# Optimization experiments

Hardware: AMD Instinct MI355X
Metric: run time of the kernel (lower is better)

The kernel has to match this reference:

```python
import jax, jax.numpy as jnp
import numpy as np

ALPHA = 0.2
SIGMA_REC = 0.15
B, T, N, IN, OUT, MASK_LEN = 256, 750, 512, 6, 2, 250


def setup_inputs() -> dict:
    key = jax.random.key(0)
    k_u, k_noise, k_rec, k_in, k_out, k_mask = jax.random.split(key, 6)
    noise_scale = np.sqrt(2.0 * ALPHA * SIGMA_REC ** 2).astype(np.float32)
    return {
        "u": jax.random.normal(k_u, (B, T, IN), dtype=jnp.float32),
        "noise": noise_scale * jax.random.normal(k_noise, (B, T, N), dtype=jnp.float32),
        "w_rec": jax.random.normal(k_rec, (N, N), dtype=jnp.float32) / np.float32(np.sqrt(N)),
        "w_in": jax.random.normal(k_in, (N, IN), dtype=jnp.float32) / np.float32(np.sqrt(IN)),
        "w_out": jax.random.normal(k_out, (OUT, N), dtype=jnp.float32) / np.float32(np.sqrt(N)),
        "mask": jnp.sort(jax.random.randint(k_mask, (MASK_LEN,), 0, T)),
    }


def _run_rnn(u, noise, w_rec, w_in):
    # u: [B,T,IN], noise: [B,T,N]; leaky ReLU RNN, t-1 update steps.
    b, t, _ = u.shape
    n = w_rec.shape[0]
    # Precompute input drive for all steps: [T-1, B, N]
    drive = jnp.einsum('bti,ni->tbn', u[:, : t - 1], w_in) + jnp.swapaxes(noise[:, : t - 1], 0, 1)

    def step(h, d):
        h_new = (1.0 - ALPHA) * h + ALPHA * jax.nn.relu(h @ w_rec.T + d)
        return h_new, h_new

    h0 = jnp.zeros((b, n), dtype=u.dtype)
    _, hs = jax.lax.scan(step, h0, drive)            # [T-1, B, N]
    states = jnp.concatenate([h0[None], hs], axis=0)  # [T, B, N]
    return jnp.swapaxes(states, 0, 1)                 # [B, T, N]


def reference(u, noise, w_rec, w_in, w_out, mask):
    states = _run_rnn(u, noise, w_rec, w_in)
    out = jnp.einsum('btn,on->bto', states, w_out)  # output_layer(states)
    return states, out[:, mask, :], out
```

## Files before the change

### kernel.cpp

```cpp
#include <hip/hip_runtime.h>
#include <hip/hip_bf16.h>


typedef __attribute__((ext_vector_type(4))) float f32x4;
typedef __attribute__((ext_vector_type(8))) short s16x8;

constexpr int BB = 256, TT = 750, NN = 512, INN = 6, OUTN = 2, MLEN = 250;
constexpr int BBLK = 16;
constexpr int NBLKS = BB / BBLK;
constexpr int WPB = 8;
constexpr int NSL = NN / WPB;
constexpr int NREG = 46;
constexpr int NLDSF = 18;
constexpr int HBYTES = BBLK * NN * 2;
constexpr int WOFF = HBYTES;
constexpr int SMEM_BYTES = WOFF + WPB * NLDSF * 1024;
constexpr int DRVELTS = NBLKS * WPB * 64 * 16;

__device__ __forceinline__ unsigned short f2bf(float f) {
    unsigned v = __float_as_uint(f);
    v += 0x7fffu + ((v >> 16) & 1u);
    return (unsigned short)(v >> 16);
}
__device__ __forceinline__ float bf2f(unsigned short h) {
    return __uint_as_float(((unsigned)h) << 16);
}

__global__ __launch_bounds__(256)
void drive_kernel(const float* __restrict__ u, const float* __restrict__ noise,
                  const float* __restrict__ w_in, unsigned short* __restrict__ drv)
{
    int gid = blockIdx.x * 256 + threadIdx.x;
    int t = gid >> 13;
    if (t >= TT - 1) return;
    int lane = gid & 63, w = (gid >> 6) & 7, blk = (gid >> 9) & 15;
    int qq = lane >> 4, lr = lane & 15;

    float wv[4][INN];
    #pragma unroll
    for (int tt = 0; tt < 4; ++tt) {
        int n = w * NSL + 16 * tt + lr;
        #pragma unroll
        for (int i = 0; i < INN; ++i) wv[tt][i] = w_in[n * INN + i];
    }
    alignas(16) unsigned short o[16];
    #pragma unroll
    for (int r = 0; r < 4; ++r) {
        int b = blk * BBLK + 4 * qq + r;
        const float* up = u + ((size_t)b * TT + t) * INN;
        float uv[INN];
        #pragma unroll
        for (int i = 0; i < INN; ++i) uv[i] = up[i];
        const float* np = noise + ((size_t)b * TT + t) * NN;
        #pragma unroll
        for (int tt = 0; tt < 4; ++tt) {
            int n = w * NSL + 16 * tt + lr;
            float d = np[n];
            #pragma unroll
            for (int i = 0; i < INN; ++i) d += uv[i] * wv[tt][i];
            o[tt * 4 + r] = f2bf(d);
        }
    }
    s16x8* dst = (s16x8*)(drv + (size_t)gid * 16);
    dst[0] = *(const s16x8*)&o[0];
    dst[1] = *(const s16x8*)&o[8];
}

__global__ __launch_bounds__(512, 2)
void rnn_scan_kernel(const float* __restrict__ w_rec,
                     const unsigned short* __restrict__ drv,
                     float* __restrict__ states)
{
    extern __shared__ char smem[];
    const int tid = threadIdx.x;
    const int w = tid >> 6, lane = tid & 63;
    const int qq = lane >> 4, lr = lane & 15, p7 = lr & 7;
    const int blk = blockIdx.x;
    const int bg = blk * BBLK;

    s16x8 breg[NREG];
    #pragma unroll
    for (int tt = 0; tt < 4; ++tt) {
        #pragma unroll
        for (int kk = 0; kk < 16; ++kk) {
            const int f = tt * 16 + kk;
            const int n = w * NSL + 16 * tt + lr;
            const float* p = w_rec + (size_t)n * NN + 32 * kk + 8 * qq;
            f32x4 x0 = *(const f32x4*)p;
            f32x4 x1 = *(const f32x4*)(p + 4);
            union { s16x8 v; unsigned short s[8]; } fr;
            #pragma unroll
            for (int j = 0; j < 4; ++j) { fr.s[j] = f2bf(x0[j]); fr.s[4+j] = f2bf(x1[j]); }
            if (f < NREG) breg[f] = fr.v;
            else *(s16x8*)(smem + WOFF + (w * NLDSF + (f - NREG)) * 1024 + lane * 16) = fr.v;
        }
    }
    for (int i = tid; i < HBYTES / 4; i += 512) ((unsigned*)smem)[i] = 0u;
    for (int i = tid; i < BBLK * NN; i += 512)
        states[(size_t)(bg + (i >> 9)) * TT * NN + (i & 511)] = 0.f;
    __syncthreads();

    float stl[16];
    #pragma unroll
    for (int i = 0; i < 16; ++i) stl[i] = 0.f;

    const int rb64 = (p7 & 4) << 4;
    const int hbase0 = lr * 1024 + ((qq ^ (p7 & 3)) << 4);
    const char* hbE = smem + hbase0 + rb64;
    const char* hbO = smem + hbase0 - rb64;
    const char* wbase = smem + WOFF + w * (NLDSF * 1024) + lane * 16;

    const int s0 = 8 * w + (lr >> 3);
    const unsigned LB = 4096u * qq + ((unsigned)(s0 ^ (4 * (qq & 1))) << 4) + 2 * (lr & 7);

    float* rowp[4];
    #pragma unroll
    for (int r = 0; r < 4; ++r)
        rowp[r] = states + ((size_t)(bg + 4 * qq + r) * TT + 1) * NN + w * NSL + lr;

    const unsigned short* dptr = drv + ((size_t)(blk * WPB + w) * 64 + lane) * 16;

    for (int s = 1; s < TT; ++s) {
        const s16x8* dp = (const s16x8*)dptr;
        s16x8 dv0 = dp[0], dv1 = dp[1];
        dptr += DRVELTS;

        f32x4 a0 = {0.f,0.f,0.f,0.f}, a1 = a0, a2 = a0, a3 = a0;
        #pragma unroll
        for (int kk = 0; kk < 16; ++kk) {
            s16x8 av = *(const s16x8*)(((kk & 1) ? hbO : hbE) + (kk << 6));
            a0 = __builtin_amdgcn_mfma_f32_16x16x32_bf16(av, breg[kk],      a0, 0,0,0);
            a1 = __builtin_amdgcn_mfma_f32_16x16x32_bf16(av, breg[16 + kk], a1, 0,0,0);
            if (kk < 14)
                a2 = __builtin_amdgcn_mfma_f32_16x16x32_bf16(av, breg[32+kk], a2, 0,0,0);
            else
                a2 = __builtin_amdgcn_mfma_f32_16x16x32_bf16(
                         av, *(const s16x8*)(wbase + ((kk - 14) << 10)), a2, 0, 0, 0);
            a3 = __builtin_amdgcn_mfma_f32_16x16x32_bf16(
                     av, *(const s16x8*)(wbase + ((2 + kk) << 10)), a3, 0, 0, 0);
        }

        union { s16x8 v; unsigned short e[8]; } U0, U1;
        U0.v = dv0; U1.v = dv1;
        const f32x4 aX[4] = {a0, a1, a2, a3};
        float hnv[4][4];
        #pragma unroll
        for (int tt = 0; tt < 4; ++tt) {
            #pragma unroll
            for (int r = 0; r < 4; ++r) {
                float d = bf2f(tt < 2 ? U0.e[tt * 4 + r] : U1.e[(tt - 2) * 4 + r]);
                float pre = aX[tt][r] + d;
                float hn = 0.8f * stl[tt * 4 + r] + 0.2f * fmaxf(pre, 0.f);
                stl[tt * 4 + r] = hn;
                hnv[tt][r] = hn;
                __builtin_nontemporal_store(hn, rowp[r] + tt * 16);
            }
        }
        unsigned pk[8];
        #pragma unroll
        for (int p = 0; p < 2; ++p)
            #pragma unroll
            for (int r = 0; r < 4; ++r) {
                __hip_bfloat162 h2 = __float22bfloat162_rn(
                    make_float2(hnv[2 * p][r], hnv[2 * p + 1][r]));
                pk[p * 4 + r] = *reinterpret_cast<unsigned*>(&h2);
            }
        #pragma unroll
        for (int r = 0; r < 4; ++r) rowp[r] += NN;

        asm volatile("s_waitcnt lgkmcnt(0)\n\ts_barrier" ::: "memory");

        #pragma unroll
        for (int tt = 0; tt < 4; ++tt) {
            #pragma unroll
            for (int r = 0; r < 4; ++r) {
                const unsigned C = (unsigned)(((2 * tt) ^ r) << 4);
                unsigned short hv = (tt & 1) ? (unsigned short)(pk[(tt >> 1) * 4 + r] >> 16)
                                             : (unsigned short)(pk[(tt >> 1) * 4 + r]);
                *(unsigned short*)(smem + ((LB ^ C) + 1024 * r)) = hv;
            }
        }
        asm volatile("s_waitcnt lgkmcnt(0)\n\ts_barrier" ::: "memory");
    }
}

__global__ __launch_bounds__(256)
void proj_kernel(const float* __restrict__ states, const float* __restrict__ w_out,
                 float* __restrict__ outf)
{
    const int wv   = (blockIdx.x * blockDim.x + threadIdx.x) >> 6;
    const int lane = threadIdx.x & 63;
    const float* sp = states + (size_t)wv * NN + lane * 8;
    const float* w0 = w_out + lane * 8;
    const float* w1 = w_out + NN + lane * 8;
    float d0 = 0.f, d1 = 0.f;
    #pragma unroll
    for (int i = 0; i < 8; ++i) {
        float sv = sp[i];
        d0 += sv * w0[i];
        d1 += sv * w1[i];
    }
    #pragma unroll
    for (int off = 32; off > 0; off >>= 1) {
        d0 += __shfl_xor(d0, off);
        d1 += __shfl_xor(d1, off);
    }
    if (lane == 0) {
        outf[(size_t)wv * 2]     = d0;
        outf[(size_t)wv * 2 + 1] = d1;
    }
}

__global__ void mask_kernel(const int* __restrict__ mask, const float* __restrict__ outf,
                            float* __restrict__ outm)
{
    int idx = blockIdx.x * blockDim.x + threadIdx.x;
    if (idx >= BB * MLEN * OUTN) return;
    int o  = idx % OUTN;
    int jm = (idx / OUTN) % MLEN;
    int b  = idx / (OUTN * MLEN);
    int t  = mask[jm];
    outm[idx] = outf[((size_t)b * TT + t) * OUTN + o];
}

extern "C" void kernel_launch(void* const* d_in, const int* in_sizes, int n_in,
                              void* d_out, int out_size, void* d_ws, size_t ws_size,
                              hipStream_t stream)
{
    (void)in_sizes; (void)n_in; (void)out_size; (void)ws_size;
    const float* u     = (const float*)d_in[0];
    const float* noise = (const float*)d_in[1];
    const float* w_rec = (const float*)d_in[2];
    const float* w_in  = (const float*)d_in[3];
    const float* w_out = (const float*)d_in[4];
    const int*   mask  = (const int*)d_in[5];

    float* states = (float*)d_out;
    float* outm   = states + (size_t)BB * TT * NN;
    float* outf   = outm + (size_t)BB * MLEN * OUTN;

    unsigned short* drvpk = (unsigned short*)d_ws;

    hipFuncSetAttribute((const void*)rnn_scan_kernel,
                        hipFuncAttributeMaxDynamicSharedMemorySize, SMEM_BYTES);

    drive_kernel<<<(TT - 1) * 32, 256, 0, stream>>>(u, noise, w_in, drvpk);
    rnn_scan_kernel<<<NBLKS, 512, SMEM_BYTES, stream>>>(w_rec, drvpk, states);
    proj_kernel<<<(BB * TT) / 4, 256, 0, stream>>>(states, w_out, outf);
    mask_kernel<<<(BB * MLEN * OUTN + 255) / 256, 256, 0, stream>>>(mask, outf, outm);
}
```

Measured before the change: 1.833 ms.

## Fuse output projection into RNN scan with per-warp partials and reduce kernel

Computes the w_out projection inside the recurrent scan from the freshly computed hidden states. Each wavefront reduces across its 16 lanes with DPP and writes per-wave partial sums to the workspace, and a small reduce kernel sums the 8 partials into the output. This removes the separate proj_kernel, which re-read the full states tensor of about 390 MB from memory. In exchange it adds ALU, DPP and store work to the serial time-step loop and needs a workspace large enough for the partials, falling back to the old path when the workspace is too small.

Measured after the change: 2.280 ms. 24.4% more time.

```diff
diff --git a/kernel.cpp b/kernel.cpp
--- a/kernel.cpp
+++ b/kernel.cpp
@@ -3,6 +3,7 @@
 
 
 typedef __attribute__((ext_vector_type(4))) float f32x4;
+typedef __attribute__((ext_vector_type(2))) float f32x2;
 typedef __attribute__((ext_vector_type(8))) short s16x8;
 
 constexpr int BB = 256, TT = 750, NN = 512, INN = 6, OUTN = 2, MLEN = 250;
@@ -16,6 +17,8 @@
 constexpr int WOFF = HBYTES;
 constexpr int SMEM_BYTES = WOFF + WPB * NLDSF * 1024;
 constexpr int DRVELTS = NBLKS * WPB * 64 * 16;
+constexpr size_t DRVTOT = (size_t)(TT - 1) * DRVELTS;
+constexpr size_t PARTN = (size_t)WPB * BB * TT * OUTN;
 
 __device__ __forceinline__ unsigned short f2bf(float f) {
     unsigned v = __float_as_uint(f);
@@ -25,6 +28,12 @@
 __device__ __forceinline__ float bf2f(unsigned short h) {
     return __uint_as_float(((unsigned)h) << 16);
 }
+
+#define DPPRED(v)                                                                 \
+    v += __int_as_float(__builtin_amdgcn_mov_dpp(__float_as_int(v), 0x128, 0xF, 0xF, false)); \
+    v += __int_as_float(__builtin_amdgcn_mov_dpp(__float_as_int(v), 0x124, 0xF, 0xF, false)); \
+    v += __int_as_float(__builtin_amdgcn_mov_dpp(__float_as_int(v), 0x122, 0xF, 0xF, false)); \
+    v += __int_as_float(__builtin_amdgcn_mov_dpp(__float_as_int(v), 0x121, 0xF, 0xF, false));
 
 __global__ __launch_bounds__(256)
 void drive_kernel(const float* __restrict__ u, const float* __restrict__ noise,
@@ -66,10 +75,12 @@
     dst[1] = *(const s16x8*)&o[8];
 }
 
+template<bool FUSE>
 __global__ __launch_bounds__(512, 2)
 void rnn_scan_kernel(const float* __restrict__ w_rec,
                      const unsigned short* __restrict__ drv,
-                     float* __restrict__ states)
+                     const float* __restrict__ w_out,
+                     float* __restrict__ states, float* __restrict__ part)
 {
     extern __shared__ char smem[];
     const int tid = threadIdx.x;
@@ -95,6 +106,15 @@
             else *(s16x8*)(smem + WOFF + (w * NLDSF + (f - NREG)) * 1024 + lane * 16) = fr.v;
         }
     }
+    float wo[8];
+    if (FUSE) {
+        #pragma unroll
+        for (int tt = 0; tt < 4; ++tt) {
+            int n = w * NSL + 16 * tt + lr;
+            wo[tt * 2]     = w_out[n];
+            wo[tt * 2 + 1] = w_out[NN + n];
+        }
+    }
     for (int i = tid; i < HBYTES / 4; i += 512) ((unsigned*)smem)[i] = 0u;
     for (int i = tid; i < BBLK * NN; i += 512)
         states[(size_t)(bg + (i >> 9)) * TT * NN + (i & 511)] = 0.f;
@@ -117,6 +137,8 @@
     #pragma unroll
     for (int r = 0; r < 4; ++r)
         rowp[r] = states + ((size_t)(bg + 4 * qq + r) * TT + 1) * NN + w * NSL + lr;
+
+    float* ppart = part + (((size_t)w * BB + bg + 4 * qq) * TT + 1) * OUTN;
 
     const unsigned short* dptr = drv + ((size_t)(blk * WPB + w) * 64 + lane) * 16;
 
@@ -143,28 +165,30 @@
         union { s16x8 v; unsigned short e[8]; } U0, U1;
         U0.v = dv0; U1.v = dv1;
         const f32x4 aX[4] = {a0, a1, a2, a3};
-        float hnv[4][4];
-        #pragma unroll
-        for (int tt = 0; tt < 4; ++tt) {
+        unsigned pk[8];
+        float po[8];
+        #pragma unroll
+        for (int i = 0; i < 8; ++i) po[i] = 0.f;
+        #pragma unroll
+        for (int p = 0; p < 2; ++p) {
             #pragma unroll
             for (int r = 0; r < 4; ++r) {
-                float d = bf2f(tt < 2 ? U0.e[tt * 4 + r] : U1.e[(tt - 2) * 4 + r]);
-                float pre = aX[tt][r] + d;
-                float hn = 0.8f * stl[tt * 4 + r] + 0.2f * fmaxf(pre, 0.f);
-                stl[tt * 4 + r] = hn;
-                hnv[tt][r] = hn;
-                __builtin_nontemporal_store(hn, rowp[r] + tt * 16);
+                float dE = bf2f(p == 0 ? U0.e[r]     : U1.e[r]);
+                float dO = bf2f(p == 0 ? U0.e[4 + r] : U1.e[4 + r]);
+                float hE = 0.8f * stl[(2*p)*4 + r]   + 0.2f * fmaxf(aX[2*p][r]   + dE, 0.f);
+                float hO = 0.8f * stl[(2*p+1)*4 + r] + 0.2f * fmaxf(aX[2*p+1][r] + dO, 0.f);
+                stl[(2*p)*4 + r] = hE;
+                stl[(2*p+1)*4 + r] = hO;
+                __builtin_nontemporal_store(hE, rowp[r] + (2*p) * 16);
+                __builtin_nontemporal_store(hO, rowp[r] + (2*p+1) * 16);
+                __hip_bfloat162 h2 = __float22bfloat162_rn(make_float2(hE, hO));
+                pk[p * 4 + r] = *reinterpret_cast<unsigned*>(&h2);
+                if (FUSE) {
+                    po[2*r]   += hE * wo[4*p]     + hO * wo[4*p + 2];
+                    po[2*r+1] += hE * wo[4*p + 1] + hO * wo[4*p + 3];
+                }
             }
         }
-        unsigned pk[8];
-        #pragma unroll
-        for (int p = 0; p < 2; ++p)
-            #pragma unroll
-            for (int r = 0; r < 4; ++r) {
-                __hip_bfloat162 h2 = __float22bfloat162_rn(
-                    make_float2(hnv[2 * p][r], hnv[2 * p + 1][r]));
-                pk[p * 4 + r] = *reinterpret_cast<unsigned*>(&h2);
-            }
         #pragma unroll
         for (int r = 0; r < 4; ++r) rowp[r] += NN;
 
@@ -180,8 +204,33 @@
                 *(unsigned short*)(smem + ((LB ^ C) + 1024 * r)) = hv;
             }
         }
+        if (FUSE) {
+            #pragma unroll
+            for (int i = 0; i < 8; ++i) { DPPRED(po[i]) }
+            if (lr == 0) {
+                #pragma unroll
+                for (int r = 0; r < 4; ++r) {
+                    f32x2 pr = {po[2*r], po[2*r+1]};
+                    __builtin_nontemporal_store(pr, (f32x2*)(ppart + (size_t)r * TT * OUTN));
+                }
+            }
+            ppart += OUTN;
+        }
         asm volatile("s_waitcnt lgkmcnt(0)\n\ts_barrier" ::: "memory");
     }
+}
+
+__global__ __launch_bounds__(256)
+void reduce_kernel(const float* __restrict__ part, float* __restrict__ outf)
+{
+    int idx = blockIdx.x * 256 + threadIdx.x;
+    if (idx >= BB * TT * OUTN) return;
+    float s = 0.f;
+    if ((idx >> 1) % TT != 0) {
+        #pragma unroll
+        for (int w = 0; w < WPB; ++w) s += part[(size_t)w * BB * TT * OUTN + idx];
+    }
+    outf[idx] = s;
 }
 
 __global__ __launch_bounds__(256)
@@ -227,7 +276,7 @@
                               void* d_out, int out_size, void* d_ws, size_t ws_size,
                               hipStream_t stream)
 {
-    (void)in_sizes; (void)n_in; (void)out_size; (void)ws_size;
+    (void)in_sizes; (void)n_in; (void)out_size;
     const float* u     = (const float*)d_in[0];
     const float* noise = (const float*)d_in[1];
     const float* w_rec = (const float*)d_in[2];
@@ -240,12 +289,23 @@
     float* outf   = outm + (size_t)BB * MLEN * OUTN;
 
     unsigned short* drvpk = (unsigned short*)d_ws;
-
-    hipFuncSetAttribute((const void*)rnn_scan_kernel,
-                        hipFuncAttributeMaxDynamicSharedMemorySize, SMEM_BYTES);
+    float* part = (float*)(drvpk + DRVTOT);
+    const bool fuse = ws_size >= DRVTOT * 2 + PARTN * 4;
+
+    (void)hipFuncSetAttribute((const void*)rnn_scan_kernel<true>,
+                              hipFuncAttributeMaxDynamicSharedMemorySize, SMEM_BYTES);
+    (void)hipFuncSetAttribute((const void*)rnn_scan_kernel<false>,
+                              hipFuncAttributeMaxDynamicSharedMemorySize, SMEM_BYTES);
 
     drive_kernel<<<(TT - 1) * 32, 256, 0, stream>>>(u, noise, w_in, drvpk);
-    rnn_scan_kernel<<<NBLKS, 512, SMEM_BYTES, stream>>>(w_rec, drvpk, states);
-    proj_kernel<<<(BB * TT) / 4, 256, 0, stream>>>(states, w_out, outf);
+    if (fuse) {
+        rnn_scan_kernel<true><<<NBLKS, 512, SMEM_BYTES, stream>>>(
+            w_rec, drvpk, w_out, states, part);
+        reduce_kernel<<<(BB * TT * OUTN + 255) / 256, 256, 0, stream>>>(part, outf);
+    } else {
+        rnn_scan_kernel<false><<<NBLKS, 512, SMEM_BYTES, stream>>>(
+            w_rec, drvpk, w_out, states, part);
+        proj_kernel<<<(BB * TT) / 4, 256, 0, stream>>>(states, w_out, outf);
+    }
     mask_kernel<<<(BB * MLEN * OUTN + 255) / 256, 256, 0, stream>>>(mask, outf, outm);
 }
```

## Swap MFMA operand roles so each lane holds contiguous neuron outputs

Applied to the files above, without the earlier changes.

The A and B operands of the recurrent MFMA are swapped, so each lane's accumulator now holds four consecutive neurons for one batch row instead of four batch rows for one neuron. This lets the state writeback use one 16-byte nontemporal store per tile instead of four scalar strided stores, and the bf16 hidden-state writes to LDS become 8-byte stores instead of scattered 2-byte stores. The drive kernel's output mapping is changed to match the new lane layout and loads noise as float4 vectors. The risk lies in the new LDS swizzle addressing, which must stay consistent with the A-fragment read pattern. There is also a chance of new bank conflicts.

Result: slower. 1.967 ms (+7.3%).

```diff
diff --git a/kernel.cpp b/kernel.cpp
--- a/kernel.cpp
+++ b/kernel.cpp
@@ -4,6 +4,7 @@
 
 typedef __attribute__((ext_vector_type(4))) float f32x4;
 typedef __attribute__((ext_vector_type(8))) short s16x8;
+typedef __attribute__((ext_vector_type(2))) unsigned u32x2;
 
 constexpr int BB = 256, TT = 750, NN = 512, INN = 6, OUTN = 2, MLEN = 250;
 constexpr int BBLK = 16;
@@ -35,29 +36,25 @@
     if (t >= TT - 1) return;
     int lane = gid & 63, w = (gid >> 6) & 7, blk = (gid >> 9) & 15;
     int qq = lane >> 4, lr = lane & 15;
-
-    float wv[4][INN];
+    int b = blk * BBLK + lr;
+
+    float uv[INN];
+    const float* up = u + ((size_t)b * TT + t) * INN;
+    #pragma unroll
+    for (int i = 0; i < INN; ++i) uv[i] = up[i];
+
+    const float* np = noise + ((size_t)b * TT + t) * NN;
+    alignas(16) unsigned short o[16];
     #pragma unroll
     for (int tt = 0; tt < 4; ++tt) {
-        int n = w * NSL + 16 * tt + lr;
-        #pragma unroll
-        for (int i = 0; i < INN; ++i) wv[tt][i] = w_in[n * INN + i];
-    }
-    alignas(16) unsigned short o[16];
-    #pragma unroll
-    for (int r = 0; r < 4; ++r) {
-        int b = blk * BBLK + 4 * qq + r;
-        const float* up = u + ((size_t)b * TT + t) * INN;
-        float uv[INN];
-        #pragma unroll
-        for (int i = 0; i < INN; ++i) uv[i] = up[i];
-        const float* np = noise + ((size_t)b * TT + t) * NN;
-        #pragma unroll
-        for (int tt = 0; tt < 4; ++tt) {
-            int n = w * NSL + 16 * tt + lr;
-            float d = np[n];
+        const int n0 = w * NSL + 16 * tt + 4 * qq;
+        f32x4 nz = *(const f32x4*)(np + n0);
+        #pragma unroll
+        for (int r = 0; r < 4; ++r) {
+            float d = nz[r];
+            const float* wi = w_in + (n0 + r) * INN;
             #pragma unroll
-            for (int i = 0; i < INN; ++i) d += uv[i] * wv[tt][i];
+            for (int i = 0; i < INN; ++i) d += uv[i] * wi[i];
             o[tt * 4 + r] = f2bf(d);
         }
     }
@@ -110,13 +107,10 @@
     const char* hbO = smem + hbase0 - rb64;
     const char* wbase = smem + WOFF + w * (NLDSF * 1024) + lane * 16;
 
-    const int s0 = 8 * w + (lr >> 3);
-    const unsigned LB = 4096u * qq + ((unsigned)(s0 ^ (4 * (qq & 1))) << 4) + 2 * (lr & 7);
-
-    float* rowp[4];
-    #pragma unroll
-    for (int r = 0; r < 4; ++r)
-        rowp[r] = states + ((size_t)(bg + 4 * qq + r) * TT + 1) * NN + w * NSL + lr;
+    const int s2 = 8 * w + (qq >> 1);
+    const unsigned LB2 = (unsigned)(lr * 1024 + 8 * (qq & 1));
+
+    float* sp = states + ((size_t)(bg + lr) * TT + 1) * NN + w * NSL;
 
     const unsigned short* dptr = drv + ((size_t)(blk * WPB + w) * 64 + lane) * 16;
 
@@ -128,57 +122,49 @@
         f32x4 a0 = {0.f,0.f,0.f,0.f}, a1 = a0, a2 = a0, a3 = a0;
         #pragma unroll
         for (int kk = 0; kk < 16; ++kk) {
-            s16x8 av = *(const s16x8*)(((kk & 1) ? hbO : hbE) + (kk << 6));
-            a0 = __builtin_amdgcn_mfma_f32_16x16x32_bf16(av, breg[kk],      a0, 0,0,0);
-            a1 = __builtin_amdgcn_mfma_f32_16x16x32_bf16(av, breg[16 + kk], a1, 0,0,0);
+            s16x8 hv = *(const s16x8*)(((kk & 1) ? hbO : hbE) + (kk << 6));
+            a0 = __builtin_amdgcn_mfma_f32_16x16x32_bf16(breg[kk],      hv, a0, 0,0,0);
+            a1 = __builtin_amdgcn_mfma_f32_16x16x32_bf16(breg[16 + kk], hv, a1, 0,0,0);
             if (kk < 14)
-                a2 = __builtin_amdgcn_mfma_f32_16x16x32_bf16(av, breg[32+kk], a2, 0,0,0);
+                a2 = __builtin_amdgcn_mfma_f32_16x16x32_bf16(breg[32+kk], hv, a2, 0,0,0);
             else
                 a2 = __builtin_amdgcn_mfma_f32_16x16x32_bf16(
-                         av, *(const s16x8*)(wbase + ((kk - 14) << 10)), a2, 0, 0, 0);
+                         *(const s16x8*)(wbase + ((kk - 14) << 10)), hv, a2, 0, 0, 0);
             a3 = __builtin_amdgcn_mfma_f32_16x16x32_bf16(
-                     av, *(const s16x8*)(wbase + ((2 + kk) << 10)), a3, 0, 0, 0);
+                     *(const s16x8*)(wbase + ((2 + kk) << 10)), hv, a3, 0, 0, 0);
         }
 
         union { s16x8 v; unsigned short e[8]; } U0, U1;
         U0.v = dv0; U1.v = dv1;
         const f32x4 aX[4] = {a0, a1, a2, a3};
-        float hnv[4][4];
+        unsigned pk[8];
         #pragma unroll
         for (int tt = 0; tt < 4; ++tt) {
+            float h_[4];
             #pragma unroll
             for (int r = 0; r < 4; ++r) {
                 float d = bf2f(tt < 2 ? U0.e[tt * 4 + r] : U1.e[(tt - 2) * 4 + r]);
                 float pre = aX[tt][r] + d;
                 float hn = 0.8f * stl[tt * 4 + r] + 0.2f * fmaxf(pre, 0.f);
                 stl[tt * 4 + r] = hn;
-                hnv[tt][r] = hn;
-                __builtin_nontemporal_store(hn, rowp[r] + tt * 16);
+                h_[r] = hn;
             }
-        }
-        unsigned pk[8];
-        #pragma unroll
-        for (int p = 0; p < 2; ++p)
-            #pragma unroll
-            for (int r = 0; r < 4; ++r) {
-                __hip_bfloat162 h2 = __float22bfloat162_rn(
-                    make_float2(hnv[2 * p][r], hnv[2 * p + 1][r]));
-                pk[p * 4 + r] = *reinterpret_cast<unsigned*>(&h2);
-            }
-        #pragma unroll
-        for (int r = 0; r < 4; ++r) rowp[r] += NN;
+            f32x4 hv4 = {h_[0], h_[1], h_[2], h_[3]};
+            __builtin_nontemporal_store(hv4, (f32x4*)(sp + 16 * tt + 4 * qq));
+            __hip_bfloat162 p01 = __float22bfloat162_rn(make_float2(h_[0], h_[1]));
+            __hip_bfloat162 p23 = __float22bfloat162_rn(make_float2(h_[2], h_[3]));
+            pk[2 * tt]     = *reinterpret_cast<unsigned*>(&p01);
+            pk[2 * tt + 1] = *reinterpret_cast<unsigned*>(&p23);
+        }
+        sp += NN;
 
         asm volatile("s_waitcnt lgkmcnt(0)\n\ts_barrier" ::: "memory");
 
         #pragma unroll
         for (int tt = 0; tt < 4; ++tt) {
-            #pragma unroll
-            for (int r = 0; r < 4; ++r) {
-                const unsigned C = (unsigned)(((2 * tt) ^ r) << 4);
-                unsigned short hv = (tt & 1) ? (unsigned short)(pk[(tt >> 1) * 4 + r] >> 16)
-                                             : (unsigned short)(pk[(tt >> 1) * 4 + r]);
-                *(unsigned short*)(smem + ((LB ^ C) + 1024 * r)) = hv;
-            }
+            const unsigned ad = LB2 + (unsigned)((((s2 + 2 * tt) ^ p7)) << 4);
+            u32x2 wv = {pk[2 * tt], pk[2 * tt + 1]};
+            *(u32x2*)(smem + ad) = wv;
         }
         asm volatile("s_waitcnt lgkmcnt(0)\n\ts_barrier" ::: "memory");
     }
@@ -241,8 +227,8 @@
 
     unsigned short* drvpk = (unsigned short*)d_ws;
 
-    hipFuncSetAttribute((const void*)rnn_scan_kernel,
-                        hipFuncAttributeMaxDynamicSharedMemorySize, SMEM_BYTES);
+    (void)hipFuncSetAttribute((const void*)rnn_scan_kernel,
+                              hipFuncAttributeMaxDynamicSharedMemorySize, SMEM_BYTES);
 
     drive_kernel<<<(TT - 1) * 32, 256, 0, stream>>>(u, noise, w_in, drvpk);
     rnn_scan_kernel<<<NBLKS, 512, SMEM_BYTES, stream>>>(w_rec, drvpk, states);
```
